# Kernel optimization log

Measured on AMD Instinct MI355X. Metric: run time of the kernel, lower is better.

The kernel has to match this reference:

```python
import jax, jax.numpy as jnp
import numpy as np

B, S, W = 32, 128, 20
WV, CV = 50000, 128
WD, CE = 300, 50
KS = (2, 3, 4, 5)
NF = 64
TOTF = NF * len(KS)
CF = 300
H = 512
L = 9
LP = L + 2
START, END = L, L + 1
NEG = -10000.0


def setup_inputs():
    key = jax.random.key(0)
    ks = jax.random.split(key, 40)
    def nrm(i, shape, scale=0.1):
        return jax.random.normal(ks[i], shape, dtype=jnp.float32) * scale
    inp = {}
    inp['token_ids'] = jax.random.randint(ks[0], (B, S), 0, WV)
    inp['char_ids'] = jax.random.randint(ks[1], (B, S, W), 0, CV)
    lens = jnp.sort(jax.random.randint(ks[2], (B,), S // 2, S + 1))[::-1]
    inp['lens'] = lens.astype(jnp.int32)
    inp['labels'] = jax.random.randint(ks[3], (B, S), 0, L)
    inp['word_embed'] = nrm(4, (WV, WD))
    inp['char_embed'] = nrm(5, (CV, CE))
    for j, k in enumerate(KS):
        inp['conv_w%d' % k] = nrm(6 + j, (k, CE, NF))
        inp['conv_b%d' % k] = nrm(10 + j, (NF,))
    inp['ff_w'] = nrm(14, (CF, TOTF))
    inp['ff_b'] = nrm(15, (CF,))
    inp['wgate_w'] = nrm(16, (WD, WD))
    inp['cgate_w'] = nrm(17, (CF, CF))
    inp['gate_w'] = nrm(18, (WD, WD))
    inp['wih_f'] = nrm(19, (4 * H, WD))
    inp['whh_f'] = nrm(20, (4 * H, H))
    inp['b_f'] = nrm(21, (4 * H,))
    inp['wih_b'] = nrm(22, (4 * H, WD))
    inp['whh_b'] = nrm(23, (4 * H, H))
    inp['b_b'] = nrm(24, (4 * H,))
    inp['out_w'] = nrm(25, (L, 2 * H))
    inp['out_b'] = nrm(26, (L,))
    inp['trn'] = nrm(27, (LP, LP))
    return inp


def _char_cnn(char_ids, char_embed, convs):
    x = char_embed[char_ids.reshape(-1, W)]  # [B*S, W, CE]
    feats = []
    for w, b in convs:
        y = jax.lax.conv_general_dilated(x, w, (1,), 'VALID',
                                         dimension_numbers=('NWC', 'WIO', 'NWC')) + b
        feats.append(jnp.max(jax.nn.relu(y), axis=1))  # max over time -> [B*S, NF]
    return jnp.concatenate(feats, axis=1)  # [B*S, TOTF]


def _run_lstm(x, mask, wih, whh, b, reverse):
    # x [B,S,D], mask bool [B,S]; padded steps freeze state and emit zeros (packed-seq semantics)
    xg = jnp.einsum('bsd,gd->bsg', x, wih) + b  # [B,S,4H]
    xg_t = jnp.swapaxes(xg, 0, 1)               # [S,B,4H]
    m_t = jnp.swapaxes(mask, 0, 1)[..., None]   # [S,B,1]
    h0 = jnp.zeros((x.shape[0], H), x.dtype)
    def step(carry, inp):
        h, c = carry
        g_t, m = inp
        g = g_t + h @ whh.T
        i, f, gg, o = jnp.split(g, 4, axis=-1)  # torch gate order i,f,g,o
        cn = jax.nn.sigmoid(f) * c + jax.nn.sigmoid(i) * jnp.tanh(gg)
        hn = jax.nn.sigmoid(o) * jnp.tanh(cn)
        h = jnp.where(m, hn, h)
        c = jnp.where(m, cn, c)
        return (h, c), jnp.where(m, hn, 0.0)
    _, out = jax.lax.scan(step, (h0, h0), (xg_t, m_t), reverse=reverse)
    return jnp.swapaxes(out, 0, 1)  # [B,S,H]


def _crf_norm(logits, mask, trn):
    # logits [B,S,LP]; trn[i,j] = score(prev=j -> next=i)
    alpha = logits[:, 0] + trn[:, START][None, :]
    lt = jnp.swapaxes(logits, 0, 1)[1:]                 # [S-1,B,LP]
    mt = jnp.swapaxes(mask, 0, 1)[1:][..., None]        # [S-1,B,1]
    def step(alpha, inp):
        lg, m = inp
        new = jax.scipy.special.logsumexp(alpha[:, None, :] + trn[None], axis=2) + lg
        return jnp.where(m, new, alpha), None
    alpha, _ = jax.lax.scan(step, alpha, (lt, mt))
    return jax.scipy.special.logsumexp(alpha + trn[END][None, :], axis=1)


def _crf_gold(logits, labels, lens, mask, trn):
    fm = mask.astype(logits.dtype)
    emit = jnp.take_along_axis(logits, labels[..., None], axis=2)[..., 0]
    emit = jnp.sum(emit * fm, axis=1)
    trans = trn[labels[:, 1:], labels[:, :-1]] * fm[:, 1:]
    first = trn[labels[:, 0], START]
    last_lab = jnp.take_along_axis(labels, (lens - 1)[:, None], axis=1)[:, 0]
    return emit + jnp.sum(trans, axis=1) + first + trn[END, last_lab]


def reference(token_ids, char_ids, lens, labels, word_embed, char_embed,
              conv_w2, conv_b2, conv_w3, conv_b3, conv_w4, conv_b4, conv_w5, conv_b5,
              ff_w, ff_b, wgate_w, cgate_w, gate_w,
              wih_f, whh_f, b_f, wih_b, whh_b, b_b, out_w, out_b, trn):
    word_in = word_embed[token_ids]                               # [B,S,WD]
    convs = [(conv_w2, conv_b2), (conv_w3, conv_b3), (conv_w4, conv_b4), (conv_w5, conv_b5)]
    ch = _char_cnn(char_ids, char_embed, convs)                   # [B*S,TOTF]
    char_in = (ch @ ff_w.T + ff_b).reshape(B, S, CF)              # CharCNNFF output
    g = jax.nn.sigmoid(jnp.tanh(word_in @ wgate_w.T + char_in @ cgate_w.T) @ gate_w.T)
    feats = g * word_in + (1.0 - g) * char_in                     # gated fusion (dropout = eval identity)
    mask = jnp.arange(S)[None, :] < lens[:, None]                 # [B,S] bool
    hf = _run_lstm(feats, mask, wih_f, whh_f, b_f, False)
    hb = _run_lstm(feats, mask, wih_b, whh_b, b_b, True)
    lstm_out = jnp.concatenate([hf, hb], axis=-1)                 # [B,S,2H]
    logits = lstm_out @ out_w.T + out_b                           # [B,S,L]
    pads = jnp.full((B, S, 2), NEG, logits.dtype)
    logits = jnp.concatenate([logits, pads], axis=2)              # pad_logits -> [B,S,LP]
    norm = _crf_norm(logits, mask, trn)
    gold = _crf_gold(logits, labels, lens, mask, trn)
    loglik = gold - norm
    return (loglik, logits)
```

## Files before the change

kernel.cpp:

```cpp
#include <hip/hip_runtime.h>

#define NB    32
#define SEQ   128
#define WCH   20
#define CED   50
#define NFLT  64
#define WDIM  300
#define HD    512
#define NWORD 4096
#define LPAD  11
#define NEGV  -10000.0f
#define LSTM_BLOCKS 16

typedef float f32x4 __attribute__((ext_vector_type(4)));
typedef float f32x16 __attribute__((ext_vector_type(16)));
typedef __bf16 bf16x8 __attribute__((ext_vector_type(8)));
typedef unsigned short u16x8 __attribute__((ext_vector_type(8)));
typedef unsigned short u16x4 __attribute__((ext_vector_type(4)));
typedef unsigned long long ull;

static __device__ __forceinline__ unsigned short f2bf(float f) {
  unsigned u = __builtin_bit_cast(unsigned, f);
  u += 0x7fffu + ((u >> 16) & 1u);
  return (unsigned short)(u >> 16);
}
static __device__ __forceinline__ float bf2f(unsigned short s) {
  unsigned u = ((unsigned)s) << 16;
  return __builtin_bit_cast(float, u);
}
static __device__ __forceinline__ float sigf(float x) { return 1.0f / (1.0f + expf(-x)); }

__global__ __launch_bounds__(256) void conv_kernel(
    const int* __restrict__ char_ids, const float* __restrict__ char_embed,
    const float* __restrict__ w2, const float* __restrict__ b2,
    const float* __restrict__ w3, const float* __restrict__ b3,
    const float* __restrict__ w4, const float* __restrict__ b4,
    const float* __restrict__ w5, const float* __restrict__ b5,
    float* __restrict__ ch)
{
  __shared__ __align__(16) float xT[CED][WCH];
  int wi = blockIdx.x;
  int tid = threadIdx.x;
  for (int e = tid; e < WCH * CED; e += 256) {
    int p = e / CED, c = e - p * CED;
    int cid = char_ids[wi * WCH + p];
    xT[c][p] = char_embed[cid * CED + c];
  }
  __syncthreads();
  int w = tid >> 6, f = tid & 63;
  int k = w + 2;
  int P = WCH - k + 1;
  const float* cw = (w == 0) ? w2 : (w == 1) ? w3 : (w == 2) ? w4 : w5;
  const float* cb = (w == 0) ? b2 : (w == 1) ? b3 : (w == 2) ? b4 : b5;
  float acc[19];
  #pragma unroll
  for (int p = 0; p < 19; p++) acc[p] = 0.f;
  for (int c = 0; c < CED; c++) {
    float xr[20];
    const float4* rowp = (const float4*)&xT[c][0];
    #pragma unroll
    for (int q = 0; q < 5; q++) {
      float4 v = rowp[q];
      xr[4*q+0] = v.x; xr[4*q+1] = v.y; xr[4*q+2] = v.z; xr[4*q+3] = v.w;
    }
    #pragma unroll
    for (int dw = 0; dw < 5; dw++) {
      if (dw < k) {
        float wv = cw[(dw * CED + c) * NFLT + f];
        #pragma unroll
        for (int p = 0; p < 19; p++) {
          if (p < P) acc[p] += xr[p + dw] * wv;
        }
      }
    }
  }
  float m = acc[0];
  #pragma unroll
  for (int p = 1; p < 19; p++) if (p < P) m = fmaxf(m, acc[p]);
  ch[wi * 256 + w * 64 + f] = fmaxf(0.f, m + cb[f]);
}

__global__ void gather_word_kernel(const int* __restrict__ token_ids,
                                   const float* __restrict__ word_embed,
                                   float* __restrict__ word_in)
{
  int idx = blockIdx.x * 256 + threadIdx.x;
  if (idx < NWORD * WDIM) {
    int i = idx / WDIM, c = idx - i * WDIM;
    word_in[idx] = word_embed[token_ids[i] * WDIM + c];
  }
}

__global__ __launch_bounds__(256) void gemm_bt_kernel(
    const float* __restrict__ A, const float* __restrict__ Bw,
    const float* __restrict__ bias, const float* __restrict__ Cin,
    float* __restrict__ Cout, unsigned short* __restrict__ Cbf,
    int M, int N, int K, int act, int gridN)
{
  __shared__ __align__(16) unsigned short As[128 * 32];
  __shared__ __align__(16) unsigned short Bs[128 * 32];
  int bid = blockIdx.x;
  int tm = bid / gridN, tn = bid - tm * gridN;
  int m0 = tm * 128, n0 = tn * 128;
  int tid = threadIdx.x;
  int lane = tid & 63, w = tid >> 6;
  int wr = (w >> 1) * 64, wc = (w & 1) * 64;
  f32x4 acc[4][4] = {};
  int fr = lane & 15, fk = (lane >> 4) * 8;

  for (int k0 = 0; k0 < K; k0 += 32) {
    __syncthreads();
    #pragma unroll
    for (int i = 0; i < 4; i++) {
      int idx = tid + i * 256;
      int r = idx >> 3, c4 = idx & 7;
      int kx = k0 + c4 * 4;
      int ra = m0 + r, rb = n0 + r;
      f32x4 av = {0.f,0.f,0.f,0.f}, bv = {0.f,0.f,0.f,0.f};
      if (kx < K) {
        if (ra < M) av = *(const f32x4*)&A[(size_t)ra * K + kx];
        if (rb < N) bv = *(const f32x4*)&Bw[(size_t)rb * K + kx];
      }
      u16x4 ap, bp;
      #pragma unroll
      for (int j = 0; j < 4; j++) { ap[j] = f2bf(av[j]); bp[j] = f2bf(bv[j]); }
      *(u16x4*)&As[r * 32 + c4 * 4] = ap;
      *(u16x4*)&Bs[r * 32 + c4 * 4] = bp;
    }
    __syncthreads();
    bf16x8 a[4], b[4];
    #pragma unroll
    for (int mt = 0; mt < 4; mt++)
      a[mt] = *(const bf16x8*)&As[(wr + mt * 16 + fr) * 32 + fk];
    #pragma unroll
    for (int nt = 0; nt < 4; nt++)
      b[nt] = *(const bf16x8*)&Bs[(wc + nt * 16 + fr) * 32 + fk];
    #pragma unroll
    for (int mt = 0; mt < 4; mt++)
      #pragma unroll
      for (int nt = 0; nt < 4; nt++)
        acc[mt][nt] = __builtin_amdgcn_mfma_f32_16x16x32_bf16(a[mt], b[nt], acc[mt][nt], 0, 0, 0);
  }

  #pragma unroll
  for (int mt = 0; mt < 4; mt++) {
    #pragma unroll
    for (int nt = 0; nt < 4; nt++) {
      #pragma unroll
      for (int j = 0; j < 4; j++) {
        int row = m0 + wr + mt * 16 + (lane >> 4) * 4 + j;
        int col = n0 + wc + nt * 16 + (lane & 15);
        if (row < M && col < N) {
          float v = acc[mt][nt][j];
          if (Cin)  v += Cin[(size_t)row * N + col];
          if (bias) v += bias[col];
          if (act == 1)      v = tanhf(v);
          else if (act == 2) v = sigf(v);
          if (Cbf) Cbf[(size_t)row * N + col] = f2bf(v);
          else     Cout[(size_t)row * N + col] = v;
        }
      }
    }
  }
}

__global__ void feats_kernel(const float* __restrict__ g, const float* __restrict__ word_in,
                             const float* __restrict__ char_in, float* __restrict__ feats,
                             unsigned* __restrict__ flags)
{
  if (blockIdx.x == 0 && threadIdx.x < 32)
    __hip_atomic_store(&flags[threadIdx.x], 0u, __ATOMIC_RELAXED, __HIP_MEMORY_SCOPE_AGENT);
  int idx = blockIdx.x * 256 + threadIdx.x;
  if (idx < NWORD * WDIM) {
    float gg = g[idx];
    feats[idx] = gg * word_in[idx] + (1.f - gg) * char_in[idx];
  }
}

__global__ __launch_bounds__(512, 2) void lstm_kernel(
    const unsigned short* __restrict__ xg_f, const unsigned short* __restrict__ xg_b,
    const float* __restrict__ whh_f, const float* __restrict__ whh_b,
    const int* __restrict__ lens,
    float* __restrict__ lstm_out, unsigned short* __restrict__ h_glob,
    unsigned* __restrict__ flags)
{
  int bid = blockIdx.x;
  int dir = bid >> 3, sl = bid & 7;
  int hs0 = sl << 6;
  int tid = threadIdx.x, lane = tid & 63, w = tid >> 6;
  int g = w & 3, hc = w >> 2;
  int l31 = lane & 31, le = lane >> 5;
  const unsigned short* xg = dir ? xg_b : xg_f;
  const float* whh = dir ? whh_b : whh_f;
  unsigned short* hg = h_glob + dir * (2 * NB * HD);
  unsigned* myflags = flags + dir * 16;

  bf16x8 wf[32];
  {
    const float* src = whh + (size_t)(g * HD + hs0 + hc * 32 + l31) * HD + le * 8;
    #pragma unroll
    for (int kk = 0; kk < 32; kk++) {
      u16x8 tv;
      #pragma unroll
      for (int j = 0; j < 8; j++) tv[j] = f2bf(src[kk * 16 + j]);
      wf[kk] = __builtin_bit_cast(bf16x8, tv);
    }
  }

  __shared__ __align__(16) unsigned short hS[16384];
  __shared__ float Gs[NB][260];

  int b = tid >> 4;
  int u = (tid & 15) << 2;
  int srow = tid >> 4, sq = tid & 15;
  int mylen = lens[b];
  float c4[4] = {0.f,0.f,0.f,0.f}, hp4[4] = {0.f,0.f,0.f,0.f};

  ull xq0, xq1, xq2, xq3;
  {
    int t0 = dir ? (SEQ - 1) : 0;
    const ull* xp = (const ull*)&xg[((size_t)(b * SEQ + t0)) * 2048 + hs0 + u];
    xq0 = xp[0]; xq1 = xp[128]; xq2 = xp[256]; xq3 = xp[384];
  }

  for (int s = 0; s < SEQ; s++) {
    int t = dir ? (SEQ - 1 - s) : s;
    f32x16 acc0 = {}, acc1 = {};

    if (s > 0) {
      if (tid == 0) {
        const ull* fp = (const ull*)myflags;
        for (;;) {
          ull f0 = __hip_atomic_load(fp + 0, __ATOMIC_RELAXED, __HIP_MEMORY_SCOPE_AGENT);
          ull f1 = __hip_atomic_load(fp + 1, __ATOMIC_RELAXED, __HIP_MEMORY_SCOPE_AGENT);
          ull f2 = __hip_atomic_load(fp + 2, __ATOMIC_RELAXED, __HIP_MEMORY_SCOPE_AGENT);
          ull f3 = __hip_atomic_load(fp + 3, __ATOMIC_RELAXED, __HIP_MEMORY_SCOPE_AGENT);
          unsigned mn = (unsigned)f0;
          mn = min(mn, (unsigned)(f0 >> 32));
          mn = min(mn, (unsigned)f1); mn = min(mn, (unsigned)(f1 >> 32));
          mn = min(mn, (unsigned)f2); mn = min(mn, (unsigned)(f2 >> 32));
          mn = min(mn, (unsigned)f3); mn = min(mn, (unsigned)(f3 >> 32));
          if (mn >= (unsigned)s) break;
          __builtin_amdgcn_s_sleep(1);
        }
      }
      __syncthreads();
      {
        const ull* hq = (const ull*)(hg + (s & 1) * (NB * HD));
        ull v[8];
        #pragma unroll
        for (int i = 0; i < 8; i++)
          v[i] = __hip_atomic_load(hq + srow * 128 + sq * 8 + i, __ATOMIC_RELAXED, __HIP_MEMORY_SCOPE_AGENT);
        int rs = ((srow ^ (sq & 7)) & 31) << 4;
        #pragma unroll
        for (int e2 = 0; e2 < 4; e2++) {
          int kk = 2 * sq + (e2 >> 1), e = e2 & 1;
          uint4 qv;
          qv.x = (unsigned)v[2*e2];     qv.y = (unsigned)(v[2*e2] >> 32);
          qv.z = (unsigned)v[2*e2+1];   qv.w = (unsigned)(v[2*e2+1] >> 32);
          *(uint4*)((char*)hS + (((kk * 2 + e) << 9) + rs)) = qv;
        }
      }
      __syncthreads();
      #pragma unroll
      for (int kk = 0; kk < 32; kk += 2) {
        int rs = ((l31 ^ ((kk >> 1) & 7)) & 31) << 4;
        int a0off = ((kk * 2 + le) << 9) + rs;
        int a1off = ((kk * 2 + 2 + le) << 9) + rs;
        bf16x8 a0 = *(const bf16x8*)((const char*)hS + a0off);
        bf16x8 a1 = *(const bf16x8*)((const char*)hS + a1off);
        acc0 = __builtin_amdgcn_mfma_f32_32x32x16_bf16(a0, wf[kk], acc0, 0, 0, 0);
        acc1 = __builtin_amdgcn_mfma_f32_32x32x16_bf16(a1, wf[kk+1], acc1, 0, 0, 0);
      }
    }

    #pragma unroll
    for (int r = 0; r < 16; r++) {
      int bb = (r & 3) + 8 * (r >> 2) + 4 * le;
      Gs[bb][g * 64 + hc * 32 + l31] = acc0[r] + acc1[r];
    }
    __syncthreads();

    f32x4 gi  = *(const f32x4*)&Gs[b][u];
    f32x4 gfv = *(const f32x4*)&Gs[b][64 + u];
    f32x4 ggv = *(const f32x4*)&Gs[b][128 + u];
    f32x4 gov = *(const f32x4*)&Gs[b][192 + u];
    bool mk = (t < mylen);
    f32x4 outv;
    ull hpk = 0;
    #pragma unroll
    for (int j = 0; j < 4; j++) {
      float xi = bf2f((unsigned short)(xq0 >> (16*j)));
      float xf = bf2f((unsigned short)(xq1 >> (16*j)));
      float xG = bf2f((unsigned short)(xq2 >> (16*j)));
      float xo = bf2f((unsigned short)(xq3 >> (16*j)));
      float iv = sigf(xi + gi[j]);
      float fv = sigf(xf + gfv[j]);
      float Gv = tanhf(xG + ggv[j]);
      float ov = sigf(xo + gov[j]);
      float cn = fv * c4[j] + iv * Gv;
      float hn = ov * tanhf(cn);
      if (mk) c4[j] = cn;
      float hk = mk ? hn : hp4[j];
      hp4[j] = hk;
      outv[j] = mk ? hn : 0.f;
      hpk |= ((ull)f2bf(hk)) << (16*j);
    }
    size_t obase = ((size_t)(b * SEQ + t)) * 1024 + dir * HD + hs0 + u;
    *(f32x4*)&lstm_out[obase] = outv;
    {
      ull* hd = (ull*)(hg + ((s & 1) ^ 1) * (NB * HD));
      __hip_atomic_store(&hd[(b * HD + hs0 + u) >> 2], hpk, __ATOMIC_RELAXED, __HIP_MEMORY_SCOPE_AGENT);
    }

    __syncthreads();
    if (tid == 0)
      __hip_atomic_store(&myflags[sl], (unsigned)(s + 1), __ATOMIC_RELAXED, __HIP_MEMORY_SCOPE_AGENT);

    if (s + 1 < SEQ) {
      int tn = dir ? (SEQ - 2 - s) : (s + 1);
      const ull* xp = (const ull*)&xg[((size_t)(b * SEQ + tn)) * 2048 + hs0 + u];
      xq0 = xp[0]; xq1 = xp[128]; xq2 = xp[256]; xq3 = xp[384];
    }
  }
}

__global__ __launch_bounds__(64) void logits_kernel(
    const float* __restrict__ lstm_out, const float* __restrict__ out_w,
    const float* __restrict__ out_b, float* __restrict__ lg)
{
  int rw = blockIdx.x, j = threadIdx.x;
  const float* row = lstm_out + (size_t)rw * 1024;
  float s[9];
  #pragma unroll
  for (int l = 0; l < 9; l++) s[l] = 0.f;
  for (int e = j; e < 1024; e += 64) {
    float x = row[e];
    #pragma unroll
    for (int l = 0; l < 9; l++) s[l] += x * out_w[l * 1024 + e];
  }
  #pragma unroll
  for (int l = 0; l < 9; l++) {
    #pragma unroll
    for (int off = 32; off > 0; off >>= 1) s[l] += __shfl_xor(s[l], off);
  }
  float v = NEGV;
  if (j < 9) {
    float r = (j==0)?s[0]:(j==1)?s[1]:(j==2)?s[2]:(j==3)?s[3]:(j==4)?s[4]:
              (j==5)?s[5]:(j==6)?s[6]:(j==7)?s[7]:s[8];
    v = r + out_b[j];
  }
  if (j < LPAD) lg[(size_t)rw * LPAD + j] = v;
}

__global__ __launch_bounds__(64) void crf_gold_kernel(
    const float* __restrict__ lg, const int* __restrict__ labels,
    const int* __restrict__ lens, const float* __restrict__ trn, float* __restrict__ gold)
{
  int b = blockIdx.x, j = threadIdx.x;
  int len = lens[b];
  const int* lab = labels + b * SEQ;
  const float* l0 = lg + (size_t)b * SEQ * LPAD;
  float s = 0.f;
  for (int t = j; t < SEQ; t += 64) {
    if (t < len) {
      s += l0[t * LPAD + lab[t]];
      if (t >= 1) s += trn[lab[t] * LPAD + lab[t - 1]];
    }
  }
  #pragma unroll
  for (int off = 32; off > 0; off >>= 1) s += __shfl_xor(s, off);
  if (j == 0) {
    s += trn[lab[0] * LPAD + 9];
    s += trn[10 * LPAD + lab[len - 1]];
    gold[b] = s;
  }
}

__global__ __launch_bounds__(64) void crf_norm_kernel(
    const float* __restrict__ lg, const int* __restrict__ lens,
    const float* __restrict__ trn, const float* __restrict__ gold, float* __restrict__ out_ll)
{
  int b = blockIdx.x, i = threadIdx.x;
  int len = lens[b];
  const float* l0 = lg + (size_t)b * SEQ * LPAD;
  bool act = (i < LPAD);
  float trow[LPAD];
  #pragma unroll
  for (int jj = 0; jj < LPAD; jj++) trow[jj] = act ? trn[i * LPAD + jj] : 0.f;
  float alpha = act ? (l0[i] + trow[9]) : -1e30f;

  for (int t = 1; t < SEQ; t++) {
    float vj[LPAD];
    #pragma unroll
    for (int jj = 0; jj < LPAD; jj++) vj[jj] = __shfl(alpha, jj) + trow[jj];
    float mx = vj[0];
    #pragma unroll
    for (int jj = 1; jj < LPAD; jj++) mx = fmaxf(mx, vj[jj]);
    float sum = 0.f;
    #pragma unroll
    for (int jj = 0; jj < LPAD; jj++) sum += expf(vj[jj] - mx);
    float lgv = act ? l0[t * LPAD + i] : 0.f;
    float nw = mx + logf(sum) + lgv;
    if (act && t < len) alpha = nw;
  }
  float vj[LPAD];
  #pragma unroll
  for (int jj = 0; jj < LPAD; jj++) vj[jj] = __shfl(alpha, jj) + trn[10 * LPAD + jj];
  float mx = vj[0];
  #pragma unroll
  for (int jj = 1; jj < LPAD; jj++) mx = fmaxf(mx, vj[jj]);
  float sum = 0.f;
  #pragma unroll
  for (int jj = 0; jj < LPAD; jj++) sum += expf(vj[jj] - mx);
  if (i == 0) out_ll[b] = gold[b] - (mx + logf(sum));
}

extern "C" void kernel_launch(void* const* d_in, const int* in_sizes, int n_in,
                              void* d_out, int out_size, void* d_ws, size_t ws_size,
                              hipStream_t stream)
{
  (void)in_sizes; (void)n_in; (void)out_size; (void)ws_size;
  const int*   token_ids = (const int*)d_in[0];
  const int*   char_ids  = (const int*)d_in[1];
  const int*   lens      = (const int*)d_in[2];
  const int*   labels    = (const int*)d_in[3];
  const float* word_embed= (const float*)d_in[4];
  const float* char_embed= (const float*)d_in[5];
  const float* w2 = (const float*)d_in[6];  const float* cb2 = (const float*)d_in[7];
  const float* w3 = (const float*)d_in[8];  const float* cb3 = (const float*)d_in[9];
  const float* w4 = (const float*)d_in[10]; const float* cb4 = (const float*)d_in[11];
  const float* w5 = (const float*)d_in[12]; const float* cb5 = (const float*)d_in[13];
  const float* ff_w = (const float*)d_in[14]; const float* ff_b = (const float*)d_in[15];
  const float* wgate_w = (const float*)d_in[16];
  const float* cgate_w = (const float*)d_in[17];
  const float* gate_w  = (const float*)d_in[18];
  const float* wih_f = (const float*)d_in[19]; const float* whh_f = (const float*)d_in[20];
  const float* b_f   = (const float*)d_in[21];
  const float* wih_b = (const float*)d_in[22]; const float* whh_b = (const float*)d_in[23];
  const float* b_b   = (const float*)d_in[24];
  const float* out_w = (const float*)d_in[25]; const float* out_b = (const float*)d_in[26];
  const float* trn   = (const float*)d_in[27];

  char* ws = (char*)d_ws;
  size_t off = 0;
  auto alloc = [&](size_t bytes) { void* p = ws + off; off += (bytes + 255) & ~(size_t)255; return p; };
  float* ch       = (float*)alloc((size_t)NWORD * 256 * 4);
  float* word_in  = (float*)alloc((size_t)NWORD * WDIM * 4);
  float* char_in  = (float*)alloc((size_t)NWORD * WDIM * 4);
  float* t1       = (float*)alloc((size_t)NWORD * WDIM * 4);
  float* gbuf     = (float*)alloc((size_t)NWORD * WDIM * 4);
  float* feats    = (float*)alloc((size_t)NWORD * WDIM * 4);
  unsigned short* xgf = (unsigned short*)alloc((size_t)NWORD * 2048 * 2);
  unsigned short* xgb = (unsigned short*)alloc((size_t)NWORD * 2048 * 2);
  float* lstm_o   = (float*)alloc((size_t)NWORD * 1024 * 4);
  unsigned short* hglob = (unsigned short*)alloc((size_t)2 * 2 * NB * HD * 2);
  float* gold     = (float*)alloc((size_t)NB * 4);
  unsigned* flags = (unsigned*)alloc(256);

  float* outp   = (float*)d_out;
  float* loglik = outp;
  float* logits = outp + NB;

  conv_kernel<<<NWORD, 256, 0, stream>>>(char_ids, char_embed, w2, cb2, w3, cb3, w4, cb4, w5, cb5, ch);
  gather_word_kernel<<<(NWORD * WDIM + 255) / 256, 256, 0, stream>>>(token_ids, word_embed, word_in);
  gemm_bt_kernel<<<32 * 3, 256, 0, stream>>>(ch, ff_w, ff_b, nullptr, char_in, nullptr, NWORD, 300, 256, 0, 3);
  gemm_bt_kernel<<<32 * 3, 256, 0, stream>>>(word_in, wgate_w, nullptr, nullptr, t1, nullptr, NWORD, 300, 300, 0, 3);
  gemm_bt_kernel<<<32 * 3, 256, 0, stream>>>(char_in, cgate_w, nullptr, t1, t1, nullptr, NWORD, 300, 300, 1, 3);
  gemm_bt_kernel<<<32 * 3, 256, 0, stream>>>(t1, gate_w, nullptr, nullptr, gbuf, nullptr, NWORD, 300, 300, 2, 3);
  feats_kernel<<<(NWORD * WDIM + 255) / 256, 256, 0, stream>>>(gbuf, word_in, char_in, feats, flags);
  gemm_bt_kernel<<<32 * 16, 256, 0, stream>>>(feats, wih_f, b_f, nullptr, nullptr, xgf, NWORD, 2048, 300, 0, 16);
  gemm_bt_kernel<<<32 * 16, 256, 0, stream>>>(feats, wih_b, b_b, nullptr, nullptr, xgb, NWORD, 2048, 300, 0, 16);
  {
    void* args[] = { (void*)&xgf, (void*)&xgb, (void*)&whh_f, (void*)&whh_b,
                     (void*)&lens, (void*)&lstm_o, (void*)&hglob, (void*)&flags };
    hipLaunchCooperativeKernel((void*)lstm_kernel, dim3(LSTM_BLOCKS), dim3(512), args, 0, stream);
  }
  logits_kernel<<<NWORD, 64, 0, stream>>>(lstm_o, out_w, out_b, logits);
  crf_gold_kernel<<<NB, 64, 0, stream>>>(logits, labels, lens, trn, gold);
  crf_norm_kernel<<<NB, 64, 0, stream>>>(logits, lens, trn, gold, loglik);
}
```

Before: 1.303 ms.

## Interleave forward and backward LSTM directions within each block to hide sync latency

Each of the 16 blocks now owns a 32-unit hidden slice for both directions instead of a 64-unit slice for one direction. Within a step it alternates forward and backward work, and splits the K reduction across two warp groups that are summed through shared memory. The global loads of the next direction's hidden state are issued before the current direction's gate math, so the cross-block flag wait and load latency can overlap with useful work. This doubles the register-resident recurrent weights per block and adds extra barriers and a shared-memory reduction per half-step.

```diff
diff --git a/kernel.cpp b/kernel.cpp
--- a/kernel.cpp
+++ b/kernel.cpp
@@ -184,143 +184,213 @@
     float* __restrict__ lstm_out, unsigned short* __restrict__ h_glob,
     unsigned* __restrict__ flags)
 {
-  int bid = blockIdx.x;
-  int dir = bid >> 3, sl = bid & 7;
-  int hs0 = sl << 6;
+  int sl = blockIdx.x;
+  int hs0 = sl << 5;
   int tid = threadIdx.x, lane = tid & 63, w = tid >> 6;
-  int g = w & 3, hc = w >> 2;
+  int g = w & 3, kh = w >> 2;
   int l31 = lane & 31, le = lane >> 5;
-  const unsigned short* xg = dir ? xg_b : xg_f;
-  const float* whh = dir ? whh_b : whh_f;
-  unsigned short* hg = h_glob + dir * (2 * NB * HD);
-  unsigned* myflags = flags + dir * 16;
-
-  bf16x8 wf[32];
+
+  unsigned short* hgF = h_glob;
+  unsigned short* hgB = h_glob + 2 * NB * HD;
+
+  bf16x8 wfF[16], wfB[16];
   {
-    const float* src = whh + (size_t)(g * HD + hs0 + hc * 32 + l31) * HD + le * 8;
-    #pragma unroll
-    for (int kk = 0; kk < 32; kk++) {
-      u16x8 tv;
-      #pragma unroll
-      for (int j = 0; j < 8; j++) tv[j] = f2bf(src[kk * 16 + j]);
-      wf[kk] = __builtin_bit_cast(bf16x8, tv);
+    const float* sF = whh_f + (size_t)(g * HD + hs0 + l31) * HD + kh * 256 + le * 8;
+    const float* sB = whh_b + (size_t)(g * HD + hs0 + l31) * HD + kh * 256 + le * 8;
+    #pragma unroll
+    for (int kk = 0; kk < 16; kk++) {
+      u16x8 tf_, tb_;
+      #pragma unroll
+      for (int j = 0; j < 8; j++) { tf_[j] = f2bf(sF[kk * 16 + j]); tb_[j] = f2bf(sB[kk * 16 + j]); }
+      wfF[kk] = __builtin_bit_cast(bf16x8, tf_);
+      wfB[kk] = __builtin_bit_cast(bf16x8, tb_);
     }
   }
 
   __shared__ __align__(16) unsigned short hS[16384];
-  __shared__ float Gs[NB][260];
-
-  int b = tid >> 4;
-  int u = (tid & 15) << 2;
+  __shared__ float Gs[2][NB][132];
+
+  int b = tid >> 4, up = tid & 15;
   int srow = tid >> 4, sq = tid & 15;
   int mylen = lens[b];
-  float c4[4] = {0.f,0.f,0.f,0.f}, hp4[4] = {0.f,0.f,0.f,0.f};
-
-  ull xq0, xq1, xq2, xq3;
+  float cF[2] = {0.f,0.f}, hpF[2] = {0.f,0.f};
+  float cB[2] = {0.f,0.f}, hpB[2] = {0.f,0.f};
+
+  ull hr[8];
+
+  auto stage_issue = [&](const unsigned short* hbuf) {
+    const ull* hq = (const ull*)hbuf;
+    #pragma unroll
+    for (int i = 0; i < 8; i++)
+      hr[i] = __hip_atomic_load(hq + srow * 128 + sq * 8 + i, __ATOMIC_RELAXED, __HIP_MEMORY_SCOPE_AGENT);
+  };
+  auto stage_write = [&]() {
+    int rs = ((srow ^ (sq & 7)) & 31) << 4;
+    #pragma unroll
+    for (int e2 = 0; e2 < 4; e2++) {
+      int kk = 2 * sq + (e2 >> 1), e = e2 & 1;
+      uint4 qv;
+      qv.x = (unsigned)hr[2*e2];   qv.y = (unsigned)(hr[2*e2] >> 32);
+      qv.z = (unsigned)hr[2*e2+1]; qv.w = (unsigned)(hr[2*e2+1] >> 32);
+      *(uint4*)((char*)hS + (((kk * 2 + e) << 9) + rs)) = qv;
+    }
+  };
+  auto wait_flags = [&](int base, unsigned target) {
+    if (tid == 0) {
+      const ull* fp = (const ull*)(flags + base);
+      for (;;) {
+        unsigned mn = 0xffffffffu;
+        #pragma unroll
+        for (int i = 0; i < 8; i++) {
+          ull v = __hip_atomic_load(fp + i, __ATOMIC_RELAXED, __HIP_MEMORY_SCOPE_AGENT);
+          unsigned a = (unsigned)v, bq = (unsigned)(v >> 32);
+          mn = a < mn ? a : mn; mn = bq < mn ? bq : mn;
+        }
+        if (mn >= target) break;
+        __builtin_amdgcn_s_sleep(1);
+      }
+    }
+  };
+
+  unsigned xF[4], xB[4];
   {
-    int t0 = dir ? (SEQ - 1) : 0;
-    const ull* xp = (const ull*)&xg[((size_t)(b * SEQ + t0)) * 2048 + hs0 + u];
-    xq0 = xp[0]; xq1 = xp[128]; xq2 = xp[256]; xq3 = xp[384];
+    const unsigned* pF = (const unsigned*)xg_f;
+    const unsigned* pB = (const unsigned*)xg_b;
+    size_t oF = (size_t)(b * SEQ + 0) * 1024 + (hs0 >> 1) + up;
+    size_t oB = (size_t)(b * SEQ + (SEQ - 1)) * 1024 + (hs0 >> 1) + up;
+    #pragma unroll
+    for (int g4 = 0; g4 < 4; g4++) { xF[g4] = pF[oF + g4 * 256]; xB[g4] = pB[oB + g4 * 256]; }
   }
 
   for (int s = 0; s < SEQ; s++) {
-    int t = dir ? (SEQ - 1 - s) : s;
-    f32x16 acc0 = {}, acc1 = {};
-
-    if (s > 0) {
-      if (tid == 0) {
-        const ull* fp = (const ull*)myflags;
-        for (;;) {
-          ull f0 = __hip_atomic_load(fp + 0, __ATOMIC_RELAXED, __HIP_MEMORY_SCOPE_AGENT);
-          ull f1 = __hip_atomic_load(fp + 1, __ATOMIC_RELAXED, __HIP_MEMORY_SCOPE_AGENT);
-          ull f2 = __hip_atomic_load(fp + 2, __ATOMIC_RELAXED, __HIP_MEMORY_SCOPE_AGENT);
-          ull f3 = __hip_atomic_load(fp + 3, __ATOMIC_RELAXED, __HIP_MEMORY_SCOPE_AGENT);
-          unsigned mn = (unsigned)f0;
-          mn = min(mn, (unsigned)(f0 >> 32));
-          mn = min(mn, (unsigned)f1); mn = min(mn, (unsigned)(f1 >> 32));
-          mn = min(mn, (unsigned)f2); mn = min(mn, (unsigned)(f2 >> 32));
-          mn = min(mn, (unsigned)f3); mn = min(mn, (unsigned)(f3 >> 32));
-          if (mn >= (unsigned)s) break;
-          __builtin_amdgcn_s_sleep(1);
+    int tf_ = s, tb_ = SEQ - 1 - s;
+    if (s > 0) stage_write();
+    __syncthreads();
+    {
+      f32x16 acc = {};
+      if (s > 0) {
+        #pragma unroll
+        for (int q = 0; q < 16; q++) {
+          int kk = kh * 16 + q;
+          int rs = ((l31 ^ ((kk >> 1) & 7)) & 31) << 4;
+          bf16x8 a = *(const bf16x8*)((const char*)hS + (((kk * 2 + le) << 9) + rs));
+          acc = __builtin_amdgcn_mfma_f32_32x32x16_bf16(a, wfF[q], acc, 0, 0, 0);
         }
       }
-      __syncthreads();
-      {
-        const ull* hq = (const ull*)(hg + (s & 1) * (NB * HD));
-        ull v[8];
+      #pragma unroll
+      for (int r = 0; r < 16; r++) {
+        int row = (r & 3) + 8 * (r >> 2) + 4 * le;
+        Gs[kh][row][g * 32 + l31] = acc[r];
+      }
+    }
+    if (s > 0) wait_flags(16, (unsigned)s);
+    __syncthreads();
+    if (s > 0) stage_issue(hgB + (s & 1) * (NB * HD));
+    {
+      bool mk = (tf_ < mylen);
+      float pre[4][2];
+      #pragma unroll
+      for (int g4 = 0; g4 < 4; g4++) {
+        float2 p0 = *(const float2*)&Gs[0][b][g4 * 32 + 2 * up];
+        float2 p1 = *(const float2*)&Gs[1][b][g4 * 32 + 2 * up];
+        pre[g4][0] = p0.x + p1.x; pre[g4][1] = p0.y + p1.y;
+      }
+      float2 ov; unsigned pk = 0;
+      #pragma unroll
+      for (int j = 0; j < 2; j++) {
+        float xi = bf2f((unsigned short)(xF[0] >> (16*j)));
+        float xf = bf2f((unsigned short)(xF[1] >> (16*j)));
+        float xG = bf2f((unsigned short)(xF[2] >> (16*j)));
+        float xo = bf2f((unsigned short)(xF[3] >> (16*j)));
+        float iv = sigf(xi + pre[0][j]);
+        float fv = sigf(xf + pre[1][j]);
+        float Gv = tanhf(xG + pre[2][j]);
+        float o_ = sigf(xo + pre[3][j]);
+        float cn = fv * cF[j] + iv * Gv;
+        float hh = o_ * tanhf(cn);
+        if (mk) cF[j] = cn;
+        float hk = mk ? hh : hpF[j];
+        hpF[j] = hk;
+        (&ov.x)[j] = mk ? hh : 0.f;
+        pk |= ((unsigned)f2bf(hk)) << (16*j);
+      }
+      size_t ob = (size_t)(b * SEQ + tf_) * 1024 + hs0 + 2 * up;
+      *(float2*)&lstm_out[ob] = ov;
+      unsigned* hd = (unsigned*)(hgF + ((s & 1) ^ 1) * (NB * HD));
+      __hip_atomic_store(&hd[(b * HD + hs0 + 2 * up) >> 1], pk, __ATOMIC_RELAXED, __HIP_MEMORY_SCOPE_AGENT);
+    }
+    __syncthreads();
+    if (tid == 0)
+      __hip_atomic_store(&flags[sl], (unsigned)(s + 1), __ATOMIC_RELAXED, __HIP_MEMORY_SCOPE_AGENT);
+    if (s + 1 < SEQ) {
+      const unsigned* pF = (const unsigned*)xg_f;
+      size_t oF = (size_t)(b * SEQ + (s + 1)) * 1024 + (hs0 >> 1) + up;
+      #pragma unroll
+      for (int g4 = 0; g4 < 4; g4++) xF[g4] = pF[oF + g4 * 256];
+    }
+    if (s > 0) stage_write();
+    __syncthreads();
+    {
+      f32x16 acc = {};
+      if (s > 0) {
         #pragma unroll
-        for (int i = 0; i < 8; i++)
-          v[i] = __hip_atomic_load(hq + srow * 128 + sq * 8 + i, __ATOMIC_RELAXED, __HIP_MEMORY_SCOPE_AGENT);
-        int rs = ((srow ^ (sq & 7)) & 31) << 4;
-        #pragma unroll
-        for (int e2 = 0; e2 < 4; e2++) {
-          int kk = 2 * sq + (e2 >> 1), e = e2 & 1;
-          uint4 qv;
-          qv.x = (unsigned)v[2*e2];     qv.y = (unsigned)(v[2*e2] >> 32);
-          qv.z = (unsigned)v[2*e2+1];   qv.w = (unsigned)(v[2*e2+1] >> 32);
-          *(uint4*)((char*)hS + (((kk * 2 + e) << 9) + rs)) = qv;
+        for (int q = 0; q < 16; q++) {
+          int kk = kh * 16 + q;
+          int rs = ((l31 ^ ((kk >> 1) & 7)) & 31) << 4;
+          bf16x8 a = *(const bf16x8*)((const char*)hS + (((kk * 2 + le) << 9) + rs));
+          acc = __builtin_amdgcn_mfma_f32_32x32x16_bf16(a, wfB[q], acc, 0, 0, 0);
         }
       }
-      __syncthreads();
-      #pragma unroll
-      for (int kk = 0; kk < 32; kk += 2) {
-        int rs = ((l31 ^ ((kk >> 1) & 7)) & 31) << 4;
-        int a0off = ((kk * 2 + le) << 9) + rs;
-        int a1off = ((kk * 2 + 2 + le) << 9) + rs;
-        bf16x8 a0 = *(const bf16x8*)((const char*)hS + a0off);
-        bf16x8 a1 = *(const bf16x8*)((const char*)hS + a1off);
-        acc0 = __builtin_amdgcn_mfma_f32_32x32x16_bf16(a0, wf[kk], acc0, 0, 0, 0);
-        acc1 = __builtin_amdgcn_mfma_f32_32x32x16_bf16(a1, wf[kk+1], acc1, 0, 0, 0);
-      }
-    }
-
-    #pragma unroll
-    for (int r = 0; r < 16; r++) {
-      int bb = (r & 3) + 8 * (r >> 2) + 4 * le;
-      Gs[bb][g * 64 + hc * 32 + l31] = acc0[r] + acc1[r];
-    }
-    __syncthreads();
-
-    f32x4 gi  = *(const f32x4*)&Gs[b][u];
-    f32x4 gfv = *(const f32x4*)&Gs[b][64 + u];
-    f32x4 ggv = *(const f32x4*)&Gs[b][128 + u];
-    f32x4 gov = *(const f32x4*)&Gs[b][192 + u];
-    bool mk = (t < mylen);
-    f32x4 outv;
-    ull hpk = 0;
-    #pragma unroll
-    for (int j = 0; j < 4; j++) {
-      float xi = bf2f((unsigned short)(xq0 >> (16*j)));
-      float xf = bf2f((unsigned short)(xq1 >> (16*j)));
-      float xG = bf2f((unsigned short)(xq2 >> (16*j)));
-      float xo = bf2f((unsigned short)(xq3 >> (16*j)));
-      float iv = sigf(xi + gi[j]);
-      float fv = sigf(xf + gfv[j]);
-      float Gv = tanhf(xG + ggv[j]);
-      float ov = sigf(xo + gov[j]);
-      float cn = fv * c4[j] + iv * Gv;
-      float hn = ov * tanhf(cn);
-      if (mk) c4[j] = cn;
-      float hk = mk ? hn : hp4[j];
-      hp4[j] = hk;
-      outv[j] = mk ? hn : 0.f;
-      hpk |= ((ull)f2bf(hk)) << (16*j);
-    }
-    size_t obase = ((size_t)(b * SEQ + t)) * 1024 + dir * HD + hs0 + u;
-    *(f32x4*)&lstm_out[obase] = outv;
+      #pragma unroll
+      for (int r = 0; r < 16; r++) {
+        int row = (r & 3) + 8 * (r >> 2) + 4 * le;
+        Gs[kh][row][g * 32 + l31] = acc[r];
+      }
+    }
+    if (s + 1 < SEQ) wait_flags(0, (unsigned)(s + 1));
+    __syncthreads();
+    if (s + 1 < SEQ) stage_issue(hgF + ((s + 1) & 1) * (NB * HD));
     {
-      ull* hd = (ull*)(hg + ((s & 1) ^ 1) * (NB * HD));
-      __hip_atomic_store(&hd[(b * HD + hs0 + u) >> 2], hpk, __ATOMIC_RELAXED, __HIP_MEMORY_SCOPE_AGENT);
-    }
-
+      bool mk = (tb_ < mylen);
+      float pre[4][2];
+      #pragma unroll
+      for (int g4 = 0; g4 < 4; g4++) {
+        float2 p0 = *(const float2*)&Gs[0][b][g4 * 32 + 2 * up];
+        float2 p1 = *(const float2*)&Gs[1][b][g4 * 32 + 2 * up];
+        pre[g4][0] = p0.x + p1.x; pre[g4][1] = p0.y + p1.y;
+      }
+      float2 ov; unsigned pk = 0;
+      #pragma unroll
+      for (int j = 0; j < 2; j++) {
+        float xi = bf2f((unsigned short)(xB[0] >> (16*j)));
+        float xf = bf2f((unsigned short)(xB[1] >> (16*j)));
+        float xG = bf2f((unsigned short)(xB[2] >> (16*j)));
+        float xo = bf2f((unsigned short)(xB[3] >> (16*j)));
+        float iv = sigf(xi + pre[0][j]);
+        float fv = sigf(xf + pre[1][j]);
+        float Gv = tanhf(xG + pre[2][j]);
+        float o_ = sigf(xo + pre[3][j]);
+        float cn = fv * cB[j] + iv * Gv;
+        float hh = o_ * tanhf(cn);
+        if (mk) cB[j] = cn;
+        float hk = mk ? hh : hpB[j];
+        hpB[j] = hk;
+        (&ov.x)[j] = mk ? hh : 0.f;
+        pk |= ((unsigned)f2bf(hk)) << (16*j);
+      }
+      size_t ob = (size_t)(b * SEQ + tb_) * 1024 + HD + hs0 + 2 * up;
+      *(float2*)&lstm_out[ob] = ov;
+      unsigned* hd = (unsigned*)(hgB + ((s & 1) ^ 1) * (NB * HD));
+      __hip_atomic_store(&hd[(b * HD + hs0 + 2 * up) >> 1], pk, __ATOMIC_RELAXED, __HIP_MEMORY_SCOPE_AGENT);
+    }
     __syncthreads();
     if (tid == 0)
-      __hip_atomic_store(&myflags[sl], (unsigned)(s + 1), __ATOMIC_RELAXED, __HIP_MEMORY_SCOPE_AGENT);
-
+      __hip_atomic_store(&flags[16 + sl], (unsigned)(s + 1), __ATOMIC_RELAXED, __HIP_MEMORY_SCOPE_AGENT);
     if (s + 1 < SEQ) {
-      int tn = dir ? (SEQ - 2 - s) : (s + 1);
-      const ull* xp = (const ull*)&xg[((size_t)(b * SEQ + tn)) * 2048 + hs0 + u];
-      xq0 = xp[0]; xq1 = xp[128]; xq2 = xp[256]; xq3 = xp[384];
+      const unsigned* pB = (const unsigned*)xg_b;
+      size_t oB = (size_t)(b * SEQ + (SEQ - 2 - s)) * 1024 + (hs0 >> 1) + up;
+      #pragma unroll
+      for (int g4 = 0; g4 < 4; g4++) xB[g4] = pB[oB + g4 * 256];
     }
   }
 }
```

After: 1.398 ms. 1.07x slower.
